# Kernel optimization log

Hardware: AMD Instinct MI355X
Metric: run time of the kernel (lower is better)

Reference implementation:

```python
import jax, jax.numpy as jnp
import numpy as np

B, N, L, D_IN, D = 32, 2048, 32768, 4, 64


def setup_inputs() -> dict:
    key = jax.random.key(0)
    ks = jax.random.split(key, 10)
    s = 0.05  # modest init scale for params
    return {
        "pred_node": jax.random.normal(ks[0], (B, N, D_IN), jnp.float32),
        "line_param": jax.random.normal(ks[1], (B, L, 4), jnp.float32),
        "W_embed": jax.random.normal(ks[2], (D_IN, D), jnp.float32) * s,
        "b_embed": jnp.zeros((D,), jnp.float32),
        "W1": jax.random.normal(ks[3], (2 * D, D), jnp.float32) * s,
        "b1": jnp.zeros((D,), jnp.float32),
        "W2": jax.random.normal(ks[4], (D, 4), jnp.float32) * s,
        "b2": jnp.zeros((4,), jnp.float32),
        "edge_src": jax.random.randint(ks[5], (B, L), 0, N, jnp.int32),
        "edge_dst": jax.random.randint(ks[6], (B, L), 0, N, jnp.int32),
    }


def reference(pred_node, line_param, W_embed, b_embed, W1, b1, W2, b2,
              edge_src, edge_dst):
    # node_feat_to_line_feat: Linear(4 -> d_model) over all nodes at once
    node_feat = jnp.einsum("bni,id->bnd", pred_node, W_embed) + b_embed  # (B,N,D)

    # Batched gather of node-feature pairs per edge (replaces Python loops)
    fi = jnp.take_along_axis(node_feat, edge_src[..., None].astype(jnp.int32), axis=1)  # (B,L,D)
    fj = jnp.take_along_axis(node_feat, edge_dst[..., None].astype(jnp.int32), axis=1)  # (B,L,D)
    combined = jnp.concatenate([fi, fj], axis=-1)  # (B,L,2D)

    # line_pred_head: Linear(2D->D) -> ReLU -> Dropout(eval: identity) -> Linear(D->4)
    h = jax.nn.relu(jnp.einsum("ble,ed->bld", combined, W1) + b1)
    line_pred = jnp.einsum("bld,do->blo", h, W2) + b2  # (B,L,4)

    # Cols 0,1 copied from line_param; cols 2,3 from the prediction head
    out = jnp.concatenate([line_param[..., :2], line_pred[..., 2:4]], axis=-1)
    return out
```

## Files before the change

kernel.cpp:

```cpp
#include <hip/hip_runtime.h>
#include <hip/hip_fp16.h>
#include <stdint.h>

#define B_ 32
#define N_ 2048
#define L_ 32768


__global__ __launch_bounds__(512) void prep_kernel(
    const float* __restrict__ W_embed, const float* __restrict__ b_embed,
    const float* __restrict__ W1, const float* __restrict__ b1,
    const float* __restrict__ W2, __half2* __restrict__ wh) {
    __shared__ float sacc[64][12];
    int tid = threadIdx.x;
    int d = tid & 63;
    int i = (tid >> 6) & 3;
    int half = tid >> 8;

    const float* w1base = W1 + (half ? 64 * 64 : 0);
    float acc = 0.f;
#pragma unroll
    for (int k = 0; k < 64; ++k) {
        acc = fmaf(W_embed[i * 64 + k], w1base[k * 64 + d], acc);
    }
    sacc[d][half * 4 + i] = acc;

    if (tid < 64) {
        float bb = 0.f;
#pragma unroll
        for (int k = 0; k < 64; ++k) {
            bb = fmaf(b_embed[k], W1[k * 64 + d] + W1[(64 + k) * 64 + d], bb);
        }
        sacc[d][8] = bb + b1[d];
        sacc[d][9] = W2[d * 4 + 2];
        sacc[d][10] = W2[d * 4 + 3];
    }
    __syncthreads();

    if (tid < 32) {
        int f0 = tid * 2, f1 = tid * 2 + 1;
#pragma unroll
        for (int k = 0; k < 11; ++k) {
            wh[tid * 12 + k] = __float22half2_rn(make_float2(sacc[f0][k], sacc[f1][k]));
        }
        wh[tid * 12 + 11] = __float22half2_rn(make_float2(0.f, 0.f));
    }
}

__global__ __launch_bounds__(256, 2) void edge_kernel(
    const float4* __restrict__ pred_node,
    const __half2* __restrict__ wh,
    const int* __restrict__ esrc, const int* __restrict__ edst,
    const float2* __restrict__ lp2,
    const float* __restrict__ b2,
    float4* __restrict__ out) {
    __shared__ float4 spn[N_];

    int tid = threadIdx.x;
    int bid = blockIdx.x;
    int x = bid & 7;
    int i = bid >> 3;
    int b = x + 8 * (i >> 4);
    int j = i & 15;

    const float4* pnb = pred_node + b * N_;
#pragma unroll
    for (int q = 0; q < 8; ++q) {
        int idx = tid + q * 256;
        spn[idx] = pnb[idx];
    }

    int ebase = b * L_ + j * 2048 + tid;

    int sa[8], ta[8];
    float2 lp[8];
#pragma unroll
    for (int p = 0; p < 8; ++p) {
        int e = ebase + p * 256;
        sa[p] = esrc[e];
        ta[p] = edst[e];
        lp[p] = lp2[(size_t)e * 2];
    }
    float bias2 = b2[2], bias3 = b2[3];

    __syncthreads();

    __half2 pb[8][8];
#pragma unroll
    for (int p = 0; p < 8; ++p) {
        float4 vs = spn[sa[p]];
        float4 vt = spn[ta[p]];
        pb[p][0] = __float22half2_rn(make_float2(vs.x, vs.x));
        pb[p][1] = __float22half2_rn(make_float2(vs.y, vs.y));
        pb[p][2] = __float22half2_rn(make_float2(vs.z, vs.z));
        pb[p][3] = __float22half2_rn(make_float2(vs.w, vs.w));
        pb[p][4] = __float22half2_rn(make_float2(vt.x, vt.x));
        pb[p][5] = __float22half2_rn(make_float2(vt.y, vt.y));
        pb[p][6] = __float22half2_rn(make_float2(vt.z, vt.z));
        pb[p][7] = __float22half2_rn(make_float2(vt.w, vt.w));
    }

    const __half2 zero = __float22half2_rn(make_float2(0.f, 0.f));
    __half2 acc2[8], acc3[8];
#pragma unroll
    for (int p = 0; p < 8; ++p) { acc2[p] = zero; acc3[p] = zero; }

#pragma unroll 2
    for (int c = 0; c < 8; ++c) {
#pragma unroll
        for (int f = 0; f < 4; ++f) {
            int base = (c * 4 + f) * 12;
            __half2 a0 = wh[base + 0], a1 = wh[base + 1];
            __half2 a2w = wh[base + 2], a3w = wh[base + 3];
            __half2 b0 = wh[base + 4], b1w = wh[base + 5];
            __half2 b2w = wh[base + 6], b3w = wh[base + 7];
            __half2 bs = wh[base + 8];
            __half2 c2 = wh[base + 9], c3 = wh[base + 10];
#pragma unroll
            for (int p = 0; p < 8; ++p) {
                __half2 h = bs;
                h = __hfma2(pb[p][0], a0, h);
                h = __hfma2(pb[p][1], a1, h);
                h = __hfma2(pb[p][2], a2w, h);
                h = __hfma2(pb[p][3], a3w, h);
                h = __hfma2(pb[p][4], b0, h);
                h = __hfma2(pb[p][5], b1w, h);
                h = __hfma2(pb[p][6], b2w, h);
                h = __hfma2(pb[p][7], b3w, h);
                h = __hmul2(h, __hgt2(h, zero));
                acc2[p] = __hfma2(h, c2, acc2[p]);
                acc3[p] = __hfma2(h, c3, acc3[p]);
            }
        }
    }

#pragma unroll
    for (int p = 0; p < 8; ++p) {
        int e = ebase + p * 256;
        float r2 = bias2 + __low2float(acc2[p]) + __high2float(acc2[p]);
        float r3 = bias3 + __low2float(acc3[p]) + __high2float(acc3[p]);
        out[e] = make_float4(lp[p].x, lp[p].y, r2, r3);
    }
}

extern "C" void kernel_launch(void* const* d_in, const int* in_sizes, int n_in,
                              void* d_out, int out_size, void* d_ws, size_t ws_size,
                              hipStream_t stream) {
    const float* pred_node = (const float*)d_in[0];
    const float* line_param = (const float*)d_in[1];
    const float* W_embed = (const float*)d_in[2];
    const float* b_embed = (const float*)d_in[3];
    const float* W1 = (const float*)d_in[4];
    const float* b1 = (const float*)d_in[5];
    const float* W2 = (const float*)d_in[6];
    const float* b2 = (const float*)d_in[7];
    const int* esrc = (const int*)d_in[8];
    const int* edst = (const int*)d_in[9];
    float* out = (float*)d_out;

    __half2* wh = (__half2*)d_ws;

    prep_kernel<<<1, 512, 0, stream>>>(W_embed, b_embed, W1, b1, W2, wh);
    edge_kernel<<<512, 256, 0, stream>>>((const float4*)pred_node, wh,
                                         esrc, edst,
                                         (const float2*)line_param, b2,
                                         (float4*)out);
}
```

Baseline: 113.8 us.

## Pack two edges per half2 lane instead of splitting hidden features across halves

The half2 packing changes so that each lane pair holds two different edges, with weights broadcast, instead of two hidden features for one edge. This cuts per-edge packed FMA work and leaves 4 edges per thread rather than 8. Grid size doubles to 1024 blocks and launch bounds rise to 4 blocks per SM to gain occupancy. ReLU becomes a single v_pk_max_f16, and line_param loads move to the epilogue to save registers. The trade-off is that each block reloads the 32 KB node table into shared memory twice as often per batch.

```diff
diff --git a/kernel.cpp b/kernel.cpp
--- a/kernel.cpp
+++ b/kernel.cpp
@@ -7,23 +7,34 @@
 #define L_ 32768
 
 
+static __device__ __forceinline__ __half2 pkrtz(float a, float b) {
+    return __float22half2_rn(make_float2(a, b));
+}
+
+static __device__ __forceinline__ __half2 pkmax(__half2 a, __half2 b) {
+    __half2 r;
+    asm("v_pk_max_f16 %0, %1, %2" : "=v"(r) : "v"(a), "v"(b));
+    return r;
+}
+
 __global__ __launch_bounds__(512) void prep_kernel(
     const float* __restrict__ W_embed, const float* __restrict__ b_embed,
     const float* __restrict__ W1, const float* __restrict__ b1,
     const float* __restrict__ W2, __half2* __restrict__ wh) {
-    __shared__ float sacc[64][12];
+    __shared__ float sacc[64][8];
+    __shared__ float sbias[64];
     int tid = threadIdx.x;
     int d = tid & 63;
     int i = (tid >> 6) & 3;
-    int half = tid >> 8;
+    int half_ = tid >> 8;
 
-    const float* w1base = W1 + (half ? 64 * 64 : 0);
+    const float* w1base = W1 + (half_ ? 64 * 64 : 0);
     float acc = 0.f;
 #pragma unroll
     for (int k = 0; k < 64; ++k) {
         acc = fmaf(W_embed[i * 64 + k], w1base[k * 64 + d], acc);
     }
-    sacc[d][half * 4 + i] = acc;
+    sacc[d][half_ * 4 + i] = acc;
 
     if (tid < 64) {
         float bb = 0.f;
@@ -31,23 +42,27 @@
         for (int k = 0; k < 64; ++k) {
             bb = fmaf(b_embed[k], W1[k * 64 + d] + W1[(64 + k) * 64 + d], bb);
         }
-        sacc[d][8] = bb + b1[d];
-        sacc[d][9] = W2[d * 4 + 2];
-        sacc[d][10] = W2[d * 4 + 3];
+        sbias[d] = bb + b1[d];
     }
     __syncthreads();
 
-    if (tid < 32) {
-        int f0 = tid * 2, f1 = tid * 2 + 1;
+    if (tid < 64) {
 #pragma unroll
-        for (int k = 0; k < 11; ++k) {
-            wh[tid * 12 + k] = __float22half2_rn(make_float2(sacc[f0][k], sacc[f1][k]));
+        for (int k = 0; k < 8; ++k) {
+            float v = sacc[tid][k];
+            wh[tid * 12 + k] = pkrtz(v, v);
         }
-        wh[tid * 12 + 11] = __float22half2_rn(make_float2(0.f, 0.f));
+        float bv = sbias[tid];
+        wh[tid * 12 + 8] = pkrtz(bv, bv);
+        float c2 = W2[tid * 4 + 2];
+        float c3 = W2[tid * 4 + 3];
+        wh[tid * 12 + 9] = pkrtz(c2, c2);
+        wh[tid * 12 + 10] = pkrtz(c3, c3);
+        wh[tid * 12 + 11] = pkrtz(0.f, 0.f);
     }
 }
 
-__global__ __launch_bounds__(256, 2) void edge_kernel(
+__global__ __launch_bounds__(256, 4) void edge_kernel(
     const float4* __restrict__ pred_node,
     const __half2* __restrict__ wh,
     const int* __restrict__ esrc, const int* __restrict__ edst,
@@ -60,8 +75,8 @@
     int bid = blockIdx.x;
     int x = bid & 7;
     int i = bid >> 3;
-    int b = x + 8 * (i >> 4);
-    int j = i & 15;
+    int b = x + 8 * (i >> 5);
+    int j = i & 31;
 
     const float4* pnb = pred_node + b * N_;
 #pragma unroll
@@ -70,76 +85,72 @@
         spn[idx] = pnb[idx];
     }
 
-    int ebase = b * L_ + j * 2048 + tid;
+    int ebase = b * L_ + j * 1024 + tid;
 
-    int sa[8], ta[8];
-    float2 lp[8];
+    int sa[4], ta[4];
 #pragma unroll
-    for (int p = 0; p < 8; ++p) {
+    for (int p = 0; p < 4; ++p) {
         int e = ebase + p * 256;
         sa[p] = esrc[e];
         ta[p] = edst[e];
-        lp[p] = lp2[(size_t)e * 2];
     }
     float bias2 = b2[2], bias3 = b2[3];
 
     __syncthreads();
 
-    __half2 pb[8][8];
+    __half2 px[2][8];
 #pragma unroll
-    for (int p = 0; p < 8; ++p) {
-        float4 vs = spn[sa[p]];
-        float4 vt = spn[ta[p]];
-        pb[p][0] = __float22half2_rn(make_float2(vs.x, vs.x));
-        pb[p][1] = __float22half2_rn(make_float2(vs.y, vs.y));
-        pb[p][2] = __float22half2_rn(make_float2(vs.z, vs.z));
-        pb[p][3] = __float22half2_rn(make_float2(vs.w, vs.w));
-        pb[p][4] = __float22half2_rn(make_float2(vt.x, vt.x));
-        pb[p][5] = __float22half2_rn(make_float2(vt.y, vt.y));
-        pb[p][6] = __float22half2_rn(make_float2(vt.z, vt.z));
-        pb[p][7] = __float22half2_rn(make_float2(vt.w, vt.w));
+    for (int pr = 0; pr < 2; ++pr) {
+        float4 s0 = spn[sa[2 * pr]];
+        float4 s1 = spn[sa[2 * pr + 1]];
+        float4 t0 = spn[ta[2 * pr]];
+        float4 t1 = spn[ta[2 * pr + 1]];
+        px[pr][0] = pkrtz(s0.x, s1.x);
+        px[pr][1] = pkrtz(s0.y, s1.y);
+        px[pr][2] = pkrtz(s0.z, s1.z);
+        px[pr][3] = pkrtz(s0.w, s1.w);
+        px[pr][4] = pkrtz(t0.x, t1.x);
+        px[pr][5] = pkrtz(t0.y, t1.y);
+        px[pr][6] = pkrtz(t0.z, t1.z);
+        px[pr][7] = pkrtz(t0.w, t1.w);
     }
 
-    const __half2 zero = __float22half2_rn(make_float2(0.f, 0.f));
-    __half2 acc2[8], acc3[8];
+    const __half2 zero = pkrtz(0.f, 0.f);
+    __half2 acc2[2] = {zero, zero};
+    __half2 acc3[2] = {zero, zero};
+
+#pragma unroll 4
+    for (int f = 0; f < 64; ++f) {
+        const __half2* wf = wh + f * 12;
+        __half2 w0 = wf[0], w1 = wf[1], w2w = wf[2], w3w = wf[3];
+        __half2 w4 = wf[4], w5 = wf[5], w6w = wf[6], w7w = wf[7];
+        __half2 bs = wf[8];
+        __half2 c2 = wf[9], c3 = wf[10];
 #pragma unroll
-    for (int p = 0; p < 8; ++p) { acc2[p] = zero; acc3[p] = zero; }
-
-#pragma unroll 2
-    for (int c = 0; c < 8; ++c) {
-#pragma unroll
-        for (int f = 0; f < 4; ++f) {
-            int base = (c * 4 + f) * 12;
-            __half2 a0 = wh[base + 0], a1 = wh[base + 1];
-            __half2 a2w = wh[base + 2], a3w = wh[base + 3];
-            __half2 b0 = wh[base + 4], b1w = wh[base + 5];
-            __half2 b2w = wh[base + 6], b3w = wh[base + 7];
-            __half2 bs = wh[base + 8];
-            __half2 c2 = wh[base + 9], c3 = wh[base + 10];
-#pragma unroll
-            for (int p = 0; p < 8; ++p) {
-                __half2 h = bs;
-                h = __hfma2(pb[p][0], a0, h);
-                h = __hfma2(pb[p][1], a1, h);
-                h = __hfma2(pb[p][2], a2w, h);
-                h = __hfma2(pb[p][3], a3w, h);
-                h = __hfma2(pb[p][4], b0, h);
-                h = __hfma2(pb[p][5], b1w, h);
-                h = __hfma2(pb[p][6], b2w, h);
-                h = __hfma2(pb[p][7], b3w, h);
-                h = __hmul2(h, __hgt2(h, zero));
-                acc2[p] = __hfma2(h, c2, acc2[p]);
-                acc3[p] = __hfma2(h, c3, acc3[p]);
-            }
+        for (int pr = 0; pr < 2; ++pr) {
+            __half2 h = bs;
+            h = __hfma2(px[pr][0], w0, h);
+            h = __hfma2(px[pr][1], w1, h);
+            h = __hfma2(px[pr][2], w2w, h);
+            h = __hfma2(px[pr][3], w3w, h);
+            h = __hfma2(px[pr][4], w4, h);
+            h = __hfma2(px[pr][5], w5, h);
+            h = __hfma2(px[pr][6], w6w, h);
+            h = __hfma2(px[pr][7], w7w, h);
+            h = pkmax(h, zero);
+            acc2[pr] = __hfma2(h, c2, acc2[pr]);
+            acc3[pr] = __hfma2(h, c3, acc3[pr]);
         }
     }
 
 #pragma unroll
-    for (int p = 0; p < 8; ++p) {
+    for (int p = 0; p < 4; ++p) {
         int e = ebase + p * 256;
-        float r2 = bias2 + __low2float(acc2[p]) + __high2float(acc2[p]);
-        float r3 = bias3 + __low2float(acc3[p]) + __high2float(acc3[p]);
-        out[e] = make_float4(lp[p].x, lp[p].y, r2, r3);
+        float2 lp = lp2[(size_t)e * 2];
+        int pr = p >> 1;
+        float r2 = (p & 1) ? __high2float(acc2[pr]) : __low2float(acc2[pr]);
+        float r3 = (p & 1) ? __high2float(acc3[pr]) : __low2float(acc3[pr]);
+        out[e] = make_float4(lp.x, lp.y, bias2 + r2, bias3 + r3);
     }
 }
 
@@ -161,8 +172,8 @@
     __half2* wh = (__half2*)d_ws;
 
     prep_kernel<<<1, 512, 0, stream>>>(W_embed, b_embed, W1, b1, W2, wh);
-    edge_kernel<<<512, 256, 0, stream>>>((const float4*)pred_node, wh,
-                                         esrc, edst,
-                                         (const float2*)line_param, b2,
-                                         (float4*)out);
+    edge_kernel<<<1024, 256, 0, stream>>>((const float4*)pred_node, wh,
+                                          esrc, edst,
+                                          (const float2*)line_param, b2,
+                                          (float4*)out);
 }
```

Measured after the change: 106.0 us. -6.9%, faster.
